# Kernel optimization log

Hardware: AMD Instinct MI355X
Metric: run time of the kernel (lower is better)

The kernel has to match this reference:

```python
import jax, jax.numpy as jnp
import numpy as np

B = 128
SEQ_T, SEQ_A, SEQ_V = 64, 1024, 512
D_T, D_A, D_V = 768, 256, 256
DST_LEN = SEQ_T


def setup_inputs() -> dict:
    key = jax.random.key(0)
    k1, k2, k3, k4, k5, k6 = jax.random.split(key, 6)
    return {
        "text_x": jax.random.normal(k1, (B, SEQ_T, D_T), dtype=jnp.float32),
        "audio_x": jax.random.normal(k2, (B, SEQ_A, D_A), dtype=jnp.float32),
        "video_x": jax.random.normal(k3, (B, SEQ_V, D_V), dtype=jnp.float32),
        # text_lengths in [3, DST_LEN+1] so min_len = text_lengths - 2 is in [1, DST_LEN-1]
        "text_lengths": jax.random.randint(k4, (B,), 3, DST_LEN + 2, dtype=jnp.int64 if jax.config.jax_enable_x64 else jnp.int32).astype(jnp.int32),
        "audio_lengths": jax.random.randint(k5, (B,), 1, SEQ_A + 1).astype(jnp.int32),
        "video_lengths": jax.random.randint(k6, (B,), 1, SEQ_V + 1).astype(jnp.int32),
    }


def _align(x, min_len, lengths, dst_len):
    """Vectorized version of the per-sample pad/reshape/mean loop.

    For sample b: pool_size = ceil(lengths/min_len); output row 0 is zeros;
    rows j in [1, min_len] are mean over pool_size slots of segment j-1
    (zero-padded beyond lengths); rows > min_len are zeros.
    """
    Bx, T, D = x.shape
    ps = (lengths + min_len - 1) // min_len            # [B] pool sizes (ceil)
    j = jnp.arange(dst_len)                            # [J] output rows
    t = jnp.arange(T)                                  # [T] source frames
    valid_row = (j[None, :] >= 1) & (j[None, :] <= min_len[:, None])   # [B,J]
    lo = (j[None, :] - 1) * ps[:, None]                # [B,J] segment start
    hi = j[None, :] * ps[:, None]                      # [B,J] segment end
    tt = t[None, None, :]
    W = (tt >= lo[:, :, None]) & (tt < hi[:, :, None]) & (tt < lengths[:, None, None])
    W = (W & valid_row[:, :, None]).astype(x.dtype) / ps[:, None, None].astype(x.dtype)
    return jnp.einsum('bjt,btd->bjd', W, x)            # [B, dst_len, D]


def reference(text_x, audio_x, video_x, text_lengths, audio_lengths, video_lengths):
    # forward() early-returns if all seq lens equal; here 64 != 1024 != 512 -> avg_pool
    min_len = text_lengths - 2
    audio_out = _align(audio_x, min_len, audio_lengths, DST_LEN)
    video_out = _align(video_x, min_len, video_lengths, DST_LEN)
    return (text_x, audio_out, video_out)
```

## Files before the change

### kernel.cpp

```cpp
#include <hip/hip_runtime.h>
#include <hip/hip_bf16.h>

#define BATCH   128
#define SEQ_T   64
#define SEQ_A   1024
#define SEQ_V   512
#define D_T     768
#define D_AV    256
#define DST_LEN 64

#define NB_COPY 1536

__device__ __forceinline__ void align_row(const float* __restrict__ x,
                                          const int* __restrict__ text_len,
                                          const int* __restrict__ lengths,
                                          float* __restrict__ out,
                                          int T, int idx) {
    const int b    = idx >> 6;
    const int j    = idx & 63;
    const int tid  = threadIdx.x;
    const int w    = tid >> 6;
    const int lane = tid & 63;

    const int ml  = text_len[b] - 2;
    const int len = lengths[b];

    float4 a0 = make_float4(0.f, 0.f, 0.f, 0.f);
    float4 a1 = a0, a2 = a0, a3 = a0;
    float inv = 0.f;

    if (j >= 1 && j <= ml) {
        const unsigned ps = ((unsigned)(len + ml - 1)) / (unsigned)ml;
        inv = 1.0f / (float)ps;
        const int lo = (j - 1) * (int)ps;
        int hi = j * (int)ps;
        if (hi > len) hi = len;

        const float4* __restrict__ xb =
            (const float4*)(x + (size_t)b * (size_t)T * D_AV);

        int t = lo + w;
        for (; t + 12 < hi; t += 16) {
            float4 v0 = xb[(size_t)(t     ) * 64 + lane];
            float4 v1 = xb[(size_t)(t +  4) * 64 + lane];
            float4 v2 = xb[(size_t)(t +  8) * 64 + lane];
            float4 v3 = xb[(size_t)(t + 12) * 64 + lane];
            a0.x += v0.x; a0.y += v0.y; a0.z += v0.z; a0.w += v0.w;
            a1.x += v1.x; a1.y += v1.y; a1.z += v1.z; a1.w += v1.w;
            a2.x += v2.x; a2.y += v2.y; a2.z += v2.z; a2.w += v2.w;
            a3.x += v3.x; a3.y += v3.y; a3.z += v3.z; a3.w += v3.w;
        }
        for (; t < hi; t += 4) {
            float4 v = xb[(size_t)t * 64 + lane];
            a0.x += v.x; a0.y += v.y; a0.z += v.z; a0.w += v.w;
        }
        a0.x += a1.x + a2.x + a3.x;
        a0.y += a1.y + a2.y + a3.y;
        a0.z += a1.z + a2.z + a3.z;
        a0.w += a1.w + a2.w + a3.w;
    }

    __shared__ float4 red[4][64];
    red[w][lane] = a0;
    __syncthreads();
    if (tid < 64) {
        float4 r0 = red[0][tid], r1 = red[1][tid],
               r2 = red[2][tid], r3 = red[3][tid];
        float4 s;
        s.x = (r0.x + r1.x + r2.x + r3.x) * inv;
        s.y = (r0.y + r1.y + r2.y + r3.y) * inv;
        s.z = (r0.z + r1.z + r2.z + r3.z) * inv;
        s.w = (r0.w + r1.w + r2.w + r3.w) * inv;
        float4* __restrict__ orow =
            (float4*)(out + ((size_t)b * DST_LEN + j) * D_AV);
        orow[tid] = s;
    }
}

__global__ __launch_bounds__(256)
void fused_align_kernel(const float4* __restrict__ text_in,
                        float4* __restrict__ text_out,
                        const float* __restrict__ audio_x,
                        const float* __restrict__ video_x,
                        const int* __restrict__ text_lengths,
                        const int* __restrict__ audio_lengths,
                        const int* __restrict__ video_lengths,
                        float* __restrict__ out_audio,
                        float* __restrict__ out_video) {
    const int blk = blockIdx.x;
    if (blk < NB_COPY) {
        const int base = blk * 1024 + threadIdx.x;
        #pragma unroll
        for (int k = 0; k < 4; ++k)
            text_out[base + k * 256] = text_in[base + k * 256];
    } else if (blk < NB_COPY + BATCH * DST_LEN) {
        align_row(audio_x, text_lengths, audio_lengths, out_audio,
                  SEQ_A, blk - NB_COPY);
    } else {
        align_row(video_x, text_lengths, video_lengths, out_video,
                  SEQ_V, blk - NB_COPY - BATCH * DST_LEN);
    }
}

extern "C" void kernel_launch(void* const* d_in, const int* in_sizes, int n_in,
                              void* d_out, int out_size, void* d_ws, size_t ws_size,
                              hipStream_t stream) {
    const float* text_x  = (const float*)d_in[0];
    const float* audio_x = (const float*)d_in[1];
    const float* video_x = (const float*)d_in[2];
    const int* text_lengths  = (const int*)d_in[3];
    const int* audio_lengths = (const int*)d_in[4];
    const int* video_lengths = (const int*)d_in[5];

    float* out = (float*)d_out;
    float* out_text  = out;
    float* out_audio = out_text  + (size_t)BATCH * SEQ_T * D_T;
    float* out_video = out_audio + (size_t)BATCH * DST_LEN * D_AV;

    const int blocks = NB_COPY + 2 * BATCH * DST_LEN;
    fused_align_kernel<<<blocks, 256, 0, stream>>>(
        (const float4*)text_x, (float4*)out_text,
        audio_x, video_x,
        text_lengths, audio_lengths, video_lengths,
        out_audio, out_video);
}
```

Baseline: 35.05 us.

## Split align rows across column-slice blocks with deeper unrolled accumulation

Each output row is now split across several blocks by column slice (4 for audio, 2 for video), so more threads each read time steps in parallel within a slice. The inner loop is unrolled to eight independent loads for more memory-level parallelism, and invalid rows exit early after writing zeros. The text copy blocks move after the align blocks. In exchange the grid has many more blocks, the row metadata is reloaded per block, and each block's reads cover narrower column segments.

```diff
diff --git a/kernel.cpp b/kernel.cpp
--- a/kernel.cpp
+++ b/kernel.cpp
@@ -9,71 +9,86 @@
 #define D_AV    256
 #define DST_LEN 64
 
+#define CS_A 4
+#define CS_V 2
+#define NB_A (BATCH * DST_LEN * CS_A)
+#define NB_V (BATCH * DST_LEN * CS_V)
 #define NB_COPY 1536
 
-__device__ __forceinline__ void align_row(const float* __restrict__ x,
-                                          const int* __restrict__ text_len,
-                                          const int* __restrict__ lengths,
-                                          float* __restrict__ out,
-                                          int T, int idx) {
-    const int b    = idx >> 6;
-    const int j    = idx & 63;
-    const int tid  = threadIdx.x;
-    const int w    = tid >> 6;
-    const int lane = tid & 63;
+__device__ __forceinline__ void add4(float4& a, const float4 v) {
+    a.x += v.x; a.y += v.y; a.z += v.z; a.w += v.w;
+}
+
+template<int CS>
+__device__ __forceinline__ void align_row_cs(const float* __restrict__ x,
+                                             const int* __restrict__ text_len,
+                                             const int* __restrict__ lengths,
+                                             float* __restrict__ out,
+                                             int T, int pair, int cs) {
+    constexpr int CHUNKS = 64 / CS;
+    constexpr int RSLOTS = 256 / CHUNKS;
+    const int b   = pair >> 6;
+    const int j   = pair & 63;
+    const int tid = threadIdx.x;
+    const int r   = tid / CHUNKS;
+    const int c   = tid % CHUNKS;
+    const int col = cs * CHUNKS + c;
 
     const int ml  = text_len[b] - 2;
     const int len = lengths[b];
 
-    float4 a0 = make_float4(0.f, 0.f, 0.f, 0.f);
-    float4 a1 = a0, a2 = a0, a3 = a0;
-    float inv = 0.f;
-
-    if (j >= 1 && j <= ml) {
-        const unsigned ps = ((unsigned)(len + ml - 1)) / (unsigned)ml;
-        inv = 1.0f / (float)ps;
-        const int lo = (j - 1) * (int)ps;
-        int hi = j * (int)ps;
-        if (hi > len) hi = len;
-
-        const float4* __restrict__ xb =
-            (const float4*)(x + (size_t)b * (size_t)T * D_AV);
-
-        int t = lo + w;
-        for (; t + 12 < hi; t += 16) {
-            float4 v0 = xb[(size_t)(t     ) * 64 + lane];
-            float4 v1 = xb[(size_t)(t +  4) * 64 + lane];
-            float4 v2 = xb[(size_t)(t +  8) * 64 + lane];
-            float4 v3 = xb[(size_t)(t + 12) * 64 + lane];
-            a0.x += v0.x; a0.y += v0.y; a0.z += v0.z; a0.w += v0.w;
-            a1.x += v1.x; a1.y += v1.y; a1.z += v1.z; a1.w += v1.w;
-            a2.x += v2.x; a2.y += v2.y; a2.z += v2.z; a2.w += v2.w;
-            a3.x += v3.x; a3.y += v3.y; a3.z += v3.z; a3.w += v3.w;
+    if (j < 1 || j > ml) {
+        if (cs == 0 && tid < 64) {
+            float4* __restrict__ orow =
+                (float4*)(out + ((size_t)b * DST_LEN + j) * D_AV);
+            orow[tid] = make_float4(0.f, 0.f, 0.f, 0.f);
         }
-        for (; t < hi; t += 4) {
-            float4 v = xb[(size_t)t * 64 + lane];
-            a0.x += v.x; a0.y += v.y; a0.z += v.z; a0.w += v.w;
-        }
-        a0.x += a1.x + a2.x + a3.x;
-        a0.y += a1.y + a2.y + a3.y;
-        a0.z += a1.z + a2.z + a3.z;
-        a0.w += a1.w + a2.w + a3.w;
+        return;
     }
 
-    __shared__ float4 red[4][64];
-    red[w][lane] = a0;
+    const unsigned ps = (unsigned)(len + ml - 1) / (unsigned)ml;
+    const float inv = 1.0f / (float)ps;
+    const int lo = (j - 1) * (int)ps;
+    int hi = j * (int)ps;
+    if (hi > len) hi = len;
+
+    const float4* __restrict__ xb =
+        (const float4*)(x + (size_t)b * (size_t)T * D_AV);
+
+    float4 a0 = make_float4(0.f, 0.f, 0.f, 0.f);
+    float4 a1 = a0, a2 = a0, a3 = a0, a4 = a0, a5 = a0, a6 = a0, a7 = a0;
+
+    int t = lo + r;
+    for (; t + 7 * RSLOTS < hi; t += 8 * RSLOTS) {
+        float4 v0 = xb[(size_t)(t             ) * 64 + col];
+        float4 v1 = xb[(size_t)(t + 1 * RSLOTS) * 64 + col];
+        float4 v2 = xb[(size_t)(t + 2 * RSLOTS) * 64 + col];
+        float4 v3 = xb[(size_t)(t + 3 * RSLOTS) * 64 + col];
+        float4 v4 = xb[(size_t)(t + 4 * RSLOTS) * 64 + col];
+        float4 v5 = xb[(size_t)(t + 5 * RSLOTS) * 64 + col];
+        float4 v6 = xb[(size_t)(t + 6 * RSLOTS) * 64 + col];
+        float4 v7 = xb[(size_t)(t + 7 * RSLOTS) * 64 + col];
+        add4(a0, v0); add4(a1, v1); add4(a2, v2); add4(a3, v3);
+        add4(a4, v4); add4(a5, v5); add4(a6, v6); add4(a7, v7);
+    }
+    for (; t < hi; t += RSLOTS)
+        add4(a0, xb[(size_t)t * 64 + col]);
+
+    add4(a0, a1); add4(a2, a3); add4(a4, a5); add4(a6, a7);
+    add4(a0, a2); add4(a4, a6); add4(a0, a4);
+
+    __shared__ float4 red[RSLOTS][CHUNKS];
+    red[r][c] = a0;
     __syncthreads();
-    if (tid < 64) {
-        float4 r0 = red[0][tid], r1 = red[1][tid],
-               r2 = red[2][tid], r3 = red[3][tid];
-        float4 s;
-        s.x = (r0.x + r1.x + r2.x + r3.x) * inv;
-        s.y = (r0.y + r1.y + r2.y + r3.y) * inv;
-        s.z = (r0.z + r1.z + r2.z + r3.z) * inv;
-        s.w = (r0.w + r1.w + r2.w + r3.w) * inv;
+    if (tid < CHUNKS) {
+        float4 s = make_float4(0.f, 0.f, 0.f, 0.f);
+        #pragma unroll
+        for (int rr = 0; rr < RSLOTS; ++rr)
+            add4(s, red[rr][tid]);
+        s.x *= inv; s.y *= inv; s.z *= inv; s.w *= inv;
         float4* __restrict__ orow =
             (float4*)(out + ((size_t)b * DST_LEN + j) * D_AV);
-        orow[tid] = s;
+        orow[cs * CHUNKS + tid] = s;
     }
 }
 
@@ -88,17 +103,18 @@
                         float* __restrict__ out_audio,
                         float* __restrict__ out_video) {
     const int blk = blockIdx.x;
-    if (blk < NB_COPY) {
-        const int base = blk * 1024 + threadIdx.x;
+    if (blk < NB_A) {
+        align_row_cs<CS_A>(audio_x, text_lengths, audio_lengths, out_audio,
+                           SEQ_A, blk / CS_A, blk % CS_A);
+    } else if (blk < NB_A + NB_V) {
+        const int k = blk - NB_A;
+        align_row_cs<CS_V>(video_x, text_lengths, video_lengths, out_video,
+                           SEQ_V, k / CS_V, k % CS_V);
+    } else {
+        const int base = (blk - NB_A - NB_V) * 1024 + threadIdx.x;
         #pragma unroll
         for (int k = 0; k < 4; ++k)
             text_out[base + k * 256] = text_in[base + k * 256];
-    } else if (blk < NB_COPY + BATCH * DST_LEN) {
-        align_row(audio_x, text_lengths, audio_lengths, out_audio,
-                  SEQ_A, blk - NB_COPY);
-    } else {
-        align_row(video_x, text_lengths, video_lengths, out_video,
-                  SEQ_V, blk - NB_COPY - BATCH * DST_LEN);
     }
 }
 
@@ -117,7 +133,7 @@
     float* out_audio = out_text  + (size_t)BATCH * SEQ_T * D_T;
     float* out_video = out_audio + (size_t)BATCH * DST_LEN * D_AV;
 
-    const int blocks = NB_COPY + 2 * BATCH * DST_LEN;
+    const int blocks = NB_A + NB_V + NB_COPY;
     fused_align_kernel<<<blocks, 256, 0, stream>>>(
         (const float4*)text_x, (float4*)out_text,
         audio_x, video_x,
```

New measurement: 46.42 us. +32.4%, slower.

## Repurpose idle output-row blocks to split long pooling segments across columns

Applied to the files above, without the earlier changes.

Blocks whose output row is zero (j=0 or j>min_len) now write their zeros and are then reassigned to help compute a valid row: when the pool size is large, a row's 64 float4 columns are split into 2 or 4 slices, each handled by a different block, with more time slots in flight per slice. The inner loop is unrolled to 8 independent accumulators. The aim is to balance load, since samples with short min_len otherwise leave a few blocks summing very long segments while many blocks do nothing. The cost is more index arithmetic and a reduction loop whose length depends on the split, and the speedup depends on how the input lengths are distributed.

```diff
diff --git a/kernel.cpp b/kernel.cpp
--- a/kernel.cpp
+++ b/kernel.cpp
@@ -10,70 +10,95 @@
 #define DST_LEN 64
 
 #define NB_COPY 1536
+#define NB_AV   (BATCH * DST_LEN)
+
+__device__ __forceinline__ void add4(float4& a, const float4 v) {
+    a.x += v.x; a.y += v.y; a.z += v.z; a.w += v.w;
+}
 
 __device__ __forceinline__ void align_row(const float* __restrict__ x,
                                           const int* __restrict__ text_len,
                                           const int* __restrict__ lengths,
                                           float* __restrict__ out,
                                           int T, int idx) {
-    const int b    = idx >> 6;
-    const int j    = idx & 63;
-    const int tid  = threadIdx.x;
-    const int w    = tid >> 6;
-    const int lane = tid & 63;
+    const int b   = idx >> 6;
+    const int j   = idx & 63;
+    const int tid = threadIdx.x;
 
     const int ml  = text_len[b] - 2;
     const int len = lengths[b];
 
-    float4 a0 = make_float4(0.f, 0.f, 0.f, 0.f);
-    float4 a1 = a0, a2 = a0, a3 = a0;
-    float inv = 0.f;
+    const unsigned ps = (unsigned)(len + ml - 1) / (unsigned)ml;
+    const int k  = (ps >= 128u) ? 2 : (ps >= 48u) ? 1 : 0;
+    const int NS = 1 << k;
 
+    int jj, s;
     if (j >= 1 && j <= ml) {
-        const unsigned ps = ((unsigned)(len + ml - 1)) / (unsigned)ml;
-        inv = 1.0f / (float)ps;
-        const int lo = (j - 1) * (int)ps;
-        int hi = j * (int)ps;
-        if (hi > len) hi = len;
-
-        const float4* __restrict__ xb =
-            (const float4*)(x + (size_t)b * (size_t)T * D_AV);
-
-        int t = lo + w;
-        for (; t + 12 < hi; t += 16) {
-            float4 v0 = xb[(size_t)(t     ) * 64 + lane];
-            float4 v1 = xb[(size_t)(t +  4) * 64 + lane];
-            float4 v2 = xb[(size_t)(t +  8) * 64 + lane];
-            float4 v3 = xb[(size_t)(t + 12) * 64 + lane];
-            a0.x += v0.x; a0.y += v0.y; a0.z += v0.z; a0.w += v0.w;
-            a1.x += v1.x; a1.y += v1.y; a1.z += v1.z; a1.w += v1.w;
-            a2.x += v2.x; a2.y += v2.y; a2.z += v2.z; a2.w += v2.w;
-            a3.x += v3.x; a3.y += v3.y; a3.z += v3.z; a3.w += v3.w;
+        jj = j; s = 0;
+    } else {
+        if (tid < 64) {
+            float4* __restrict__ oz =
+                (float4*)(out + ((size_t)b * DST_LEN + j) * D_AV);
+            oz[tid] = make_float4(0.f, 0.f, 0.f, 0.f);
         }
-        for (; t < hi; t += 4) {
-            float4 v = xb[(size_t)t * 64 + lane];
-            a0.x += v.x; a0.y += v.y; a0.z += v.z; a0.w += v.w;
-        }
-        a0.x += a1.x + a2.x + a3.x;
-        a0.y += a1.y + a2.y + a3.y;
-        a0.z += a1.z + a2.z + a3.z;
-        a0.w += a1.w + a2.w + a3.w;
+        if (j == 0) return;
+        s  = (j - 1) / ml;
+        jj = j - s * ml;
+        if (s >= NS) return;
     }
 
-    __shared__ float4 red[4][64];
-    red[w][lane] = a0;
+    const int cols = 64 >> k;
+    const int r    = tid >> (6 - k);
+    const int c    = tid & (cols - 1);
+    const int col  = s * cols + c;
+    const int slots = 4 << k;
+
+    const float inv = 1.0f / (float)ps;
+    const int lo = (jj - 1) * (int)ps;
+    int hi = jj * (int)ps;
+    if (hi > len) hi = len;
+
+    const float4* __restrict__ xb =
+        (const float4*)(x + (size_t)b * (size_t)T * D_AV);
+
+    float4 a0 = make_float4(0.f, 0.f, 0.f, 0.f);
+    float4 a1 = a0, a2 = a0, a3 = a0, a4 = a0, a5 = a0, a6 = a0, a7 = a0;
+
+    int t = lo + r;
+    for (; t + 7 * slots < hi; t += 8 * slots) {
+        float4 v0 = xb[(size_t)(t            ) * 64 + col];
+        float4 v1 = xb[(size_t)(t + 1 * slots) * 64 + col];
+        float4 v2 = xb[(size_t)(t + 2 * slots) * 64 + col];
+        float4 v3 = xb[(size_t)(t + 3 * slots) * 64 + col];
+        float4 v4 = xb[(size_t)(t + 4 * slots) * 64 + col];
+        float4 v5 = xb[(size_t)(t + 5 * slots) * 64 + col];
+        float4 v6 = xb[(size_t)(t + 6 * slots) * 64 + col];
+        float4 v7 = xb[(size_t)(t + 7 * slots) * 64 + col];
+        add4(a0, v0); add4(a1, v1); add4(a2, v2); add4(a3, v3);
+        add4(a4, v4); add4(a5, v5); add4(a6, v6); add4(a7, v7);
+    }
+    for (; t + slots < hi; t += 2 * slots) {
+        float4 v0 = xb[(size_t)t * 64 + col];
+        float4 v1 = xb[(size_t)(t + slots) * 64 + col];
+        add4(a0, v0); add4(a1, v1);
+    }
+    if (t < hi)
+        add4(a0, xb[(size_t)t * 64 + col]);
+
+    add4(a0, a1); add4(a2, a3); add4(a4, a5); add4(a6, a7);
+    add4(a0, a2); add4(a4, a6); add4(a0, a4);
+
+    __shared__ float4 red[256];
+    red[tid] = a0;
     __syncthreads();
-    if (tid < 64) {
-        float4 r0 = red[0][tid], r1 = red[1][tid],
-               r2 = red[2][tid], r3 = red[3][tid];
-        float4 s;
-        s.x = (r0.x + r1.x + r2.x + r3.x) * inv;
-        s.y = (r0.y + r1.y + r2.y + r3.y) * inv;
-        s.z = (r0.z + r1.z + r2.z + r3.z) * inv;
-        s.w = (r0.w + r1.w + r2.w + r3.w) * inv;
+    if (tid < cols) {
+        float4 sum = make_float4(0.f, 0.f, 0.f, 0.f);
+        for (int rr = 0; rr < slots; ++rr)
+            add4(sum, red[rr * cols + tid]);
+        sum.x *= inv; sum.y *= inv; sum.z *= inv; sum.w *= inv;
         float4* __restrict__ orow =
-            (float4*)(out + ((size_t)b * DST_LEN + j) * D_AV);
-        orow[tid] = s;
+            (float4*)(out + ((size_t)b * DST_LEN + jj) * D_AV);
+        orow[s * cols + tid] = sum;
     }
 }
 
@@ -93,12 +118,12 @@
         #pragma unroll
         for (int k = 0; k < 4; ++k)
             text_out[base + k * 256] = text_in[base + k * 256];
-    } else if (blk < NB_COPY + BATCH * DST_LEN) {
+    } else if (blk < NB_COPY + NB_AV) {
         align_row(audio_x, text_lengths, audio_lengths, out_audio,
                   SEQ_A, blk - NB_COPY);
     } else {
         align_row(video_x, text_lengths, video_lengths, out_video,
-                  SEQ_V, blk - NB_COPY - BATCH * DST_LEN);
+                  SEQ_V, blk - NB_COPY - NB_AV);
     }
 }
 
@@ -117,7 +142,7 @@
     float* out_audio = out_text  + (size_t)BATCH * SEQ_T * D_T;
     float* out_video = out_audio + (size_t)BATCH * DST_LEN * D_AV;
 
-    const int blocks = NB_COPY + 2 * BATCH * DST_LEN;
+    const int blocks = NB_COPY + 2 * NB_AV;
     fused_align_kernel<<<blocks, 256, 0, stream>>>(
         (const float4*)text_x, (float4*)out_text,
         audio_x, video_x,
```

New measurement: 30.97 us. -11.6%, faster.
